# Kernel optimization log

Measured on AMD Instinct MI355X. Metric: run time of the kernel, lower is better.

## Reference

```python
import jax, jax.numpy as jnp
import numpy as np

WBITS = 4
ABITS = 8
OBITS = 8


def fwht(x):
    """Normalized fast Walsh-Hadamard transform along the last axis (n power of 2).
    Equivalent to matmul_hadU with had_K = I, K = 1 (n = 4096 = 2^12)."""
    shape = x.shape
    n = shape[-1]
    x = x.reshape(-1, n)
    h = 1
    while h < n:
        x = x.reshape(-1, n // (2 * h), 2, h)
        a, b = x[:, :, 0, :], x[:, :, 1, :]
        x = jnp.concatenate([a + b, a - b], axis=-1).reshape(-1, n)
        h *= 2
    inv_sqrt_n = jnp.asarray(1.0 / np.sqrt(n), x.dtype)
    return (x * inv_sqrt_n).reshape(shape)


def sym_fake_quant(t, bits, axis):
    """Symmetric min-max RTN fake quantization (per-channel for weights,
    per-token for activations)."""
    qmax = jnp.asarray(2.0 ** (bits - 1) - 1.0, t.dtype)
    scale = jnp.max(jnp.abs(t), axis=axis, keepdims=True) / qmax
    scale = jnp.maximum(scale, jnp.asarray(1e-8, t.dtype))
    q = jnp.clip(jnp.round(t / scale), -qmax, qmax)
    return q * scale


def setup_inputs() -> dict:
    key = jax.random.key(0)
    k1, k2, k3 = jax.random.split(key, 3)
    B, S, DIN, DOUT = 4, 2048, 4096, 4096
    return {
        "input": jax.random.normal(k1, (B, S, DIN), dtype=jnp.float32),
        "weight": jax.random.normal(k2, (DOUT, DIN), dtype=jnp.float32) * 0.02,
        "bias": jax.random.normal(k3, (DOUT,), dtype=jnp.float32) * 0.01,
    }


def reference(input, weight, bias):
    # online full Hadamard rotation of activations
    x = fwht(input)
    # activation quant (per-token, symmetric int8 fake-quant)
    x = sym_fake_quant(x, ABITS, axis=-1)
    # weight quant (per-output-channel, symmetric int4 fake-quant)
    w = sym_fake_quant(weight, WBITS, axis=-1)
    # F.linear: x @ w.T + b
    out = jnp.einsum("bsi,oi->bso", x, w) + bias
    # output quant (per-token, symmetric int8 fake-quant)
    out = sym_fake_quant(out, OBITS, axis=-1)
    return out
```

## Files before the change

kernel.cpp:

```cpp
#include <hip/hip_runtime.h>
#include <hip/hip_bf16.h>

#define DIN 4096
#define DOUT 4096
#define NROWS 8192

typedef int i32x4 __attribute__((ext_vector_type(4)));
typedef int i32x16 __attribute__((ext_vector_type(16)));

__device__ __forceinline__ float block_absmax(float m, float* red) {
  #pragma unroll
  for (int off = 32; off > 0; off >>= 1)
    m = fmaxf(m, __shfl_down(m, off));
  const int tid = threadIdx.x;
  if ((tid & 63) == 0) red[tid >> 6] = m;
  __syncthreads();
  return fmaxf(fmaxf(red[0], red[1]), fmaxf(red[2], red[3]));
}

__global__ __launch_bounds__(256) void fwht_quant_kernel(
    const float* __restrict__ in, char* __restrict__ qx,
    float* __restrict__ sx) {
  __shared__ float lds[4352];
  __shared__ float red[4];
  const int tid = threadIdx.x;
  const size_t row = blockIdx.x;
  const int th = tid >> 4, tl = tid & 15;
  float v[16];

  const float4* src = (const float4*)(in + row * DIN);
  #pragma unroll
  for (int k = 0; k < 4; ++k) {
    float4 f = src[tid * 4 + k];
    v[4 * k + 0] = f.x; v[4 * k + 1] = f.y;
    v[4 * k + 2] = f.z; v[4 * k + 3] = f.w;
  }
  #pragma unroll
  for (int hb = 1; hb < 16; hb <<= 1)
    #pragma unroll
    for (int j = 0; j < 16; ++j)
      if (!(j & hb)) {
        float a0 = v[j], b0 = v[j | hb];
        v[j] = a0 + b0; v[j | hb] = a0 - b0;
      }
  #pragma unroll
  for (int j = 0; j < 16; ++j) lds[17 * tid + j] = v[j];
  __syncthreads();
  #pragma unroll
  for (int j = 0; j < 16; ++j) v[j] = lds[272 * th + 17 * j + tl];
  #pragma unroll
  for (int hb = 1; hb < 16; hb <<= 1)
    #pragma unroll
    for (int j = 0; j < 16; ++j)
      if (!(j & hb)) {
        float a0 = v[j], b0 = v[j | hb];
        v[j] = a0 + b0; v[j | hb] = a0 - b0;
      }
  #pragma unroll
  for (int j = 0; j < 16; ++j) lds[272 * th + 17 * j + tl] = v[j];
  __syncthreads();
  #pragma unroll
  for (int j = 0; j < 16; ++j) v[j] = lds[272 * j + 17 * th + tl];
  #pragma unroll
  for (int hb = 1; hb < 16; hb <<= 1)
    #pragma unroll
    for (int j = 0; j < 16; ++j)
      if (!(j & hb)) {
        float a0 = v[j], b0 = v[j | hb];
        v[j] = a0 + b0; v[j | hb] = a0 - b0;
      }
  float m = 0.0f;
  #pragma unroll
  for (int j = 0; j < 16; ++j) m = fmaxf(m, fabsf(v[j]));
  #pragma unroll
  for (int j = 0; j < 16; ++j) lds[272 * j + 17 * th + tl] = v[j];
  float mx = block_absmax(m, red) * 0.015625f;
  float scale = fmaxf(mx / 127.0f, 1e-8f);
  if (tid == 0) sx[row] = scale;
  const float rs = 1.0f / scale;
  char pk[16];
  #pragma unroll
  for (int j = 0; j < 16; ++j) {
    float q = fminf(fmaxf(rintf((lds[17 * tid + j] * 0.015625f) * rs), -127.f),
                    127.f);
    pk[j] = (char)q;
  }
  *(int4*)(qx + row * DIN + (size_t)tid * 16) = *(const int4*)pk;
}

__global__ __launch_bounds__(256) void wquant_kernel(
    const float* __restrict__ w, char* __restrict__ qw,
    float* __restrict__ sw) {
  __shared__ float buf[DIN];
  __shared__ float red[4];
  const int tid = threadIdx.x;
  const size_t row = blockIdx.x;
  const float4* src = (const float4*)(w + row * DIN);
  float4* b4 = (float4*)buf;
  float m = 0.0f;
  for (int i = tid; i < DIN / 4; i += 256) {
    float4 v = src[i];
    b4[i] = v;
    m = fmaxf(m, fmaxf(fmaxf(fabsf(v.x), fabsf(v.y)),
                       fmaxf(fabsf(v.z), fabsf(v.w))));
  }
  float mx = block_absmax(m, red);
  float scale = fmaxf(mx / 7.0f, 1e-8f);
  if (tid == 0) sw[row] = scale;
  char* dst = qw + row * DIN;
  const float rs = 1.0f / scale;
  for (int i0 = tid * 4; i0 < DIN; i0 += 1024) {
    char4 pk;
    float q0 = fminf(fmaxf(rintf(buf[i0 + 0] * rs), -7.f), 7.f);
    float q1 = fminf(fmaxf(rintf(buf[i0 + 1] * rs), -7.f), 7.f);
    float q2 = fminf(fmaxf(rintf(buf[i0 + 2] * rs), -7.f), 7.f);
    float q3 = fminf(fmaxf(rintf(buf[i0 + 3] * rs), -7.f), 7.f);
    pk.x = (char)q0; pk.y = (char)q1; pk.z = (char)q2; pk.w = (char)q3;
    *(char4*)(dst + i0) = pk;
  }
}

__global__ __launch_bounds__(512, 2) void gemm_kernel(
    const char* __restrict__ A,
    const char* __restrict__ Bt,
    const float* __restrict__ sx, const float* __restrict__ sw,
    const float* __restrict__ bias, float* __restrict__ out) {
  __shared__ char lds[131072];
  const int tid = threadIdx.x;
  const int lane = tid & 63;
  const int wid = tid >> 6;
  const int wr = wid >> 2;
  const int wc = wid & 3;
  const int lh = lane >> 5;
  const int l31 = lane & 31;
  int bid = blockIdx.x;
  int swz = (bid & 7) * 64 + (bid >> 3);
  const size_t row0 = (size_t)(swz >> 4) * 256;
  const size_t col0 = (size_t)(swz & 15) * 256;

  i32x16 acc[4][2] = {};
  i32x4 faA[4], faB[4];
  i32x4 fb[2][4];

#define STAGE(MAT, GROW0, KT, LBASE)                                          \
  {                                                                           \
    _Pragma("unroll")                                                         \
    for (int j = 0; j < 2; ++j) {                                             \
      int chunk = j * 8 + wid;                                                \
      int rr = chunk * 8 + (lane >> 3);                                       \
      int cc = (KT) * 128 + (((lane & 7) ^ (lane >> 3)) << 4);                \
      const char* src = (MAT) + ((GROW0) + rr) * (size_t)DIN + cc;            \
      __builtin_amdgcn_global_load_lds(                                       \
          (const __attribute__((address_space(1))) void*)src,                 \
          (__attribute__((address_space(3))) void*)(lds + (LBASE) +           \
                                                    chunk * 1024),            \
          16, 0, 0);                                                          \
    }                                                                         \
  }
#define STAGE_A(P, HALF, KT) \
  STAGE(A, row0 + (HALF) * 128, KT, (P) * 32768 + (HALF) * 16384)
#define STAGE_B(P, HALF, KT) \
  STAGE(Bt, col0 + (HALF) * 128, KT, 65536 + (P) * 32768 + (HALF) * 16384)

#define DS_FA(DST, Q, P)                                                      \
  {                                                                           \
    int ar_ = (Q) * 64 + wr * 32 + l31;                                       \
    _Pragma("unroll")                                                         \
    for (int kk = 0; kk < 4; ++kk)                                            \
      DST[kk] = *(const i32x4*)(lds + (P) * 32768 + ar_ * 128 +               \
                                (((kk * 2 + lh) ^ (ar_ & 7)) << 4));          \
  }
#define DS_FB(P)                                                              \
  {                                                                           \
    _Pragma("unroll")                                                         \
    for (int nn = 0; nn < 2; ++nn) {                                          \
      int br_ = wc * 64 + nn * 32 + l31;                                      \
      _Pragma("unroll")                                                       \
      for (int kk = 0; kk < 4; ++kk)                                          \
        fb[nn][kk] = *(const i32x4*)(lds + 65536 + (P) * 32768 + br_ * 128 +  \
                                     (((kk * 2 + lh) ^ (br_ & 7)) << 4));     \
    }                                                                         \
  }
#define MFMA8(Q, FA)                                                          \
  {                                                                           \
    __builtin_amdgcn_s_setprio(1);                                            \
    _Pragma("unroll")                                                         \
    for (int kk = 0; kk < 4; ++kk)                                            \
      _Pragma("unroll")                                                       \
      for (int nn = 0; nn < 2; ++nn)                                          \
        acc[Q][nn] = __builtin_amdgcn_mfma_i32_32x32x32_i8(                   \
            fb[nn][kk], FA[kk], acc[Q][nn], 0, 0, 0);                         \
    __builtin_amdgcn_s_setprio(0);                                            \
  }
#define BAR() __builtin_amdgcn_s_barrier()
#define SCHED0() __builtin_amdgcn_sched_barrier(0)

  STAGE_B(0, 0, 0); STAGE_B(0, 1, 0); STAGE_A(0, 0, 0); STAGE_A(0, 1, 0);
  STAGE_B(1, 0, 1); STAGE_B(1, 1, 1); STAGE_A(1, 0, 1);
  asm volatile("s_waitcnt vmcnt(6)" ::: "memory");
  BAR();
  DS_FA(faA, 0, 0);

  #pragma unroll 1
  for (int i = 0; i < 16; ++i) {
    const int a = 2 * i, b = 2 * i + 1;
    const bool nl = (i < 15);
    DS_FB(0);
    DS_FA(faB, 1, 0);
    STAGE_A(1, 1, b);
    SCHED0();
    MFMA8(0, faA);
    BAR();
    DS_FA(faA, 2, 0);
    if (nl) STAGE_B(0, 0, a + 2);
    SCHED0();
    MFMA8(1, faB);
    BAR();
    DS_FA(faB, 3, 0);
    if (nl) STAGE_B(0, 1, a + 2);
    SCHED0();
    MFMA8(2, faA);
    if (nl) { asm volatile("s_waitcnt vmcnt(4)" ::: "memory"); }
    else    { asm volatile("s_waitcnt vmcnt(0)" ::: "memory"); }
    BAR();
    DS_FA(faA, 0, 1);
    if (nl) STAGE_A(0, 0, a + 2);
    SCHED0();
    MFMA8(3, faB);
    BAR();
    DS_FB(1);
    DS_FA(faB, 1, 1);
    if (nl) STAGE_A(0, 1, a + 2);
    SCHED0();
    MFMA8(0, faA);
    BAR();
    DS_FA(faA, 2, 1);
    if (nl) STAGE_B(1, 0, b + 2);
    SCHED0();
    MFMA8(1, faB);
    BAR();
    DS_FA(faB, 3, 1);
    if (nl) STAGE_B(1, 1, b + 2);
    SCHED0();
    MFMA8(2, faA);
    if (nl) { asm volatile("s_waitcnt vmcnt(4)" ::: "memory"); }
    BAR();
    if (nl) { DS_FA(faA, 0, 0); STAGE_A(1, 0, b + 2); }
    SCHED0();
    MFMA8(3, faB);
    BAR();
  }

  #pragma unroll
  for (int q = 0; q < 4; ++q) {
    size_t gr = row0 + q * 64 + wr * 32 + l31;
    float sxr = sx[gr];
    float* orow = out + gr * DOUT;
    #pragma unroll
    for (int nn = 0; nn < 2; ++nn) {
      #pragma unroll
      for (int r4 = 0; r4 < 4; ++r4) {
        size_t gc0 = col0 + wc * 64 + nn * 32 + 8 * r4 + 4 * lh;
        float4 swv = *(const float4*)(sw + gc0);
        float4 bv = *(const float4*)(bias + gc0);
        float4 o;
        o.x = (float)acc[q][nn][r4 * 4 + 0] * (sxr * swv.x) + bv.x;
        o.y = (float)acc[q][nn][r4 * 4 + 1] * (sxr * swv.y) + bv.y;
        o.z = (float)acc[q][nn][r4 * 4 + 2] * (sxr * swv.z) + bv.z;
        o.w = (float)acc[q][nn][r4 * 4 + 3] * (sxr * swv.w) + bv.w;
        *(float4*)(orow + gc0) = o;
      }
    }
  }
#undef STAGE
#undef STAGE_A
#undef STAGE_B
#undef DS_FA
#undef DS_FB
#undef MFMA8
#undef BAR
#undef SCHED0
}

__global__ __launch_bounds__(256) void rowquant_kernel(float* __restrict__ out) {
  __shared__ float red[4];
  const int tid = threadIdx.x;
  const size_t row = blockIdx.x;
  float4* g4 = (float4*)(out + row * DOUT);
  float4 v[4];
  float m = 0.0f;
  #pragma unroll
  for (int k = 0; k < 4; ++k) {
    v[k] = g4[tid + k * 256];
    m = fmaxf(m, fmaxf(fmaxf(fabsf(v[k].x), fabsf(v[k].y)),
                       fmaxf(fabsf(v[k].z), fabsf(v[k].w))));
  }
  float mx = block_absmax(m, red);
  float scale = fmaxf(mx / 127.0f, 1e-8f);
  #pragma unroll
  for (int k = 0; k < 4; ++k) {
    float4 w = v[k];
    w.x = fminf(fmaxf(rintf(w.x / scale), -127.0f), 127.0f) * scale;
    w.y = fminf(fmaxf(rintf(w.y / scale), -127.0f), 127.0f) * scale;
    w.z = fminf(fmaxf(rintf(w.z / scale), -127.0f), 127.0f) * scale;
    w.w = fminf(fmaxf(rintf(w.w / scale), -127.0f), 127.0f) * scale;
    g4[tid + k * 256] = w;
  }
}

extern "C" void kernel_launch(void* const* d_in, const int* in_sizes, int n_in,
                              void* d_out, int out_size, void* d_ws, size_t ws_size,
                              hipStream_t stream) {
  (void)in_sizes; (void)n_in; (void)out_size; (void)ws_size;
  const float* input = (const float*)d_in[0];
  const float* weight = (const float*)d_in[1];
  const float* bias = (const float*)d_in[2];
  float* out = (float*)d_out;
  char* ws = (char*)d_ws;
  char* qx = ws;
  char* qw = ws + ((size_t)32 << 20);
  float* sx = (float*)(ws + ((size_t)48 << 20));
  float* sw = (float*)(ws + ((size_t)48 << 20) + ((size_t)32 << 10));

  fwht_quant_kernel<<<NROWS, 256, 0, stream>>>(input, qx, sx);
  wquant_kernel<<<DOUT, 256, 0, stream>>>(weight, qw, sw);
  gemm_kernel<<<512, 512, 0, stream>>>(qx, qw, sx, sw, bias, out);
  rowquant_kernel<<<NROWS, 256, 0, stream>>>(out);
}
```

Before: 256.3 us.

## Merge activation and weight quant launches; add explicit LDS waits and barriers in GEMM

The FWHT activation quantization and the weight quantization now run as one launch, with the block index choosing which path a block takes. This removes one launch and the tail gap between the two kernels. In the GEMM main loop, each sched_barrier is replaced by an explicit lgkmcnt wait plus an extra workgroup barrier before every MFMA group, so the LDS fragment reads are waited on at a partial count rather than left to the compiler. The extra barriers may add stalls, and the hand-set lgkmcnt counts must exactly match the number of outstanding LDS and scalar ops or fragments will be read before they arrive.

```diff
diff --git a/kernel.cpp b/kernel.cpp
--- a/kernel.cpp
+++ b/kernel.cpp
@@ -18,105 +18,101 @@
   return fmaxf(fmaxf(red[0], red[1]), fmaxf(red[2], red[3]));
 }
 
-__global__ __launch_bounds__(256) void fwht_quant_kernel(
-    const float* __restrict__ in, char* __restrict__ qx,
-    float* __restrict__ sx) {
+__global__ __launch_bounds__(256) void fused_quant_kernel(
+    const float* __restrict__ in, const float* __restrict__ w,
+    char* __restrict__ qx, char* __restrict__ qw,
+    float* __restrict__ sx, float* __restrict__ sw) {
   __shared__ float lds[4352];
   __shared__ float red[4];
   const int tid = threadIdx.x;
-  const size_t row = blockIdx.x;
-  const int th = tid >> 4, tl = tid & 15;
-  float v[16];
-
-  const float4* src = (const float4*)(in + row * DIN);
-  #pragma unroll
-  for (int k = 0; k < 4; ++k) {
-    float4 f = src[tid * 4 + k];
-    v[4 * k + 0] = f.x; v[4 * k + 1] = f.y;
-    v[4 * k + 2] = f.z; v[4 * k + 3] = f.w;
-  }
-  #pragma unroll
-  for (int hb = 1; hb < 16; hb <<= 1)
-    #pragma unroll
-    for (int j = 0; j < 16; ++j)
-      if (!(j & hb)) {
-        float a0 = v[j], b0 = v[j | hb];
-        v[j] = a0 + b0; v[j | hb] = a0 - b0;
-      }
-  #pragma unroll
-  for (int j = 0; j < 16; ++j) lds[17 * tid + j] = v[j];
-  __syncthreads();
-  #pragma unroll
-  for (int j = 0; j < 16; ++j) v[j] = lds[272 * th + 17 * j + tl];
-  #pragma unroll
-  for (int hb = 1; hb < 16; hb <<= 1)
-    #pragma unroll
-    for (int j = 0; j < 16; ++j)
-      if (!(j & hb)) {
-        float a0 = v[j], b0 = v[j | hb];
-        v[j] = a0 + b0; v[j | hb] = a0 - b0;
-      }
-  #pragma unroll
-  for (int j = 0; j < 16; ++j) lds[272 * th + 17 * j + tl] = v[j];
-  __syncthreads();
-  #pragma unroll
-  for (int j = 0; j < 16; ++j) v[j] = lds[272 * j + 17 * th + tl];
-  #pragma unroll
-  for (int hb = 1; hb < 16; hb <<= 1)
-    #pragma unroll
-    for (int j = 0; j < 16; ++j)
-      if (!(j & hb)) {
-        float a0 = v[j], b0 = v[j | hb];
-        v[j] = a0 + b0; v[j | hb] = a0 - b0;
-      }
-  float m = 0.0f;
-  #pragma unroll
-  for (int j = 0; j < 16; ++j) m = fmaxf(m, fabsf(v[j]));
-  #pragma unroll
-  for (int j = 0; j < 16; ++j) lds[272 * j + 17 * th + tl] = v[j];
-  float mx = block_absmax(m, red) * 0.015625f;
-  float scale = fmaxf(mx / 127.0f, 1e-8f);
-  if (tid == 0) sx[row] = scale;
-  const float rs = 1.0f / scale;
-  char pk[16];
-  #pragma unroll
-  for (int j = 0; j < 16; ++j) {
-    float q = fminf(fmaxf(rintf((lds[17 * tid + j] * 0.015625f) * rs), -127.f),
-                    127.f);
-    pk[j] = (char)q;
-  }
-  *(int4*)(qx + row * DIN + (size_t)tid * 16) = *(const int4*)pk;
-}
-
-__global__ __launch_bounds__(256) void wquant_kernel(
-    const float* __restrict__ w, char* __restrict__ qw,
-    float* __restrict__ sw) {
-  __shared__ float buf[DIN];
-  __shared__ float red[4];
-  const int tid = threadIdx.x;
-  const size_t row = blockIdx.x;
-  const float4* src = (const float4*)(w + row * DIN);
-  float4* b4 = (float4*)buf;
-  float m = 0.0f;
-  for (int i = tid; i < DIN / 4; i += 256) {
-    float4 v = src[i];
-    b4[i] = v;
-    m = fmaxf(m, fmaxf(fmaxf(fabsf(v.x), fabsf(v.y)),
-                       fmaxf(fabsf(v.z), fabsf(v.w))));
-  }
-  float mx = block_absmax(m, red);
-  float scale = fmaxf(mx / 7.0f, 1e-8f);
-  if (tid == 0) sw[row] = scale;
-  char* dst = qw + row * DIN;
-  const float rs = 1.0f / scale;
-  for (int i0 = tid * 4; i0 < DIN; i0 += 1024) {
-    char4 pk;
-    float q0 = fminf(fmaxf(rintf(buf[i0 + 0] * rs), -7.f), 7.f);
-    float q1 = fminf(fmaxf(rintf(buf[i0 + 1] * rs), -7.f), 7.f);
-    float q2 = fminf(fmaxf(rintf(buf[i0 + 2] * rs), -7.f), 7.f);
-    float q3 = fminf(fmaxf(rintf(buf[i0 + 3] * rs), -7.f), 7.f);
-    pk.x = (char)q0; pk.y = (char)q1; pk.z = (char)q2; pk.w = (char)q3;
-    *(char4*)(dst + i0) = pk;
+
+  if (blockIdx.x < NROWS) {
+    const size_t row = blockIdx.x;
+    const int th = tid >> 4, tl = tid & 15;
+    float v[16];
+    const float4* src = (const float4*)(in + row * DIN);
+    #pragma unroll
+    for (int k = 0; k < 4; ++k) {
+      float4 f = src[tid * 4 + k];
+      v[4 * k + 0] = f.x; v[4 * k + 1] = f.y;
+      v[4 * k + 2] = f.z; v[4 * k + 3] = f.w;
+    }
+    #pragma unroll
+    for (int hb = 1; hb < 16; hb <<= 1)
+      #pragma unroll
+      for (int j = 0; j < 16; ++j)
+        if (!(j & hb)) {
+          float a0 = v[j], b0 = v[j | hb];
+          v[j] = a0 + b0; v[j | hb] = a0 - b0;
+        }
+    #pragma unroll
+    for (int j = 0; j < 16; ++j) lds[17 * tid + j] = v[j];
+    __syncthreads();
+    #pragma unroll
+    for (int j = 0; j < 16; ++j) v[j] = lds[272 * th + 17 * j + tl];
+    #pragma unroll
+    for (int hb = 1; hb < 16; hb <<= 1)
+      #pragma unroll
+      for (int j = 0; j < 16; ++j)
+        if (!(j & hb)) {
+          float a0 = v[j], b0 = v[j | hb];
+          v[j] = a0 + b0; v[j | hb] = a0 - b0;
+        }
+    #pragma unroll
+    for (int j = 0; j < 16; ++j) lds[272 * th + 17 * j + tl] = v[j];
+    __syncthreads();
+    #pragma unroll
+    for (int j = 0; j < 16; ++j) v[j] = lds[272 * j + 17 * th + tl];
+    #pragma unroll
+    for (int hb = 1; hb < 16; hb <<= 1)
+      #pragma unroll
+      for (int j = 0; j < 16; ++j)
+        if (!(j & hb)) {
+          float a0 = v[j], b0 = v[j | hb];
+          v[j] = a0 + b0; v[j | hb] = a0 - b0;
+        }
+    float m = 0.0f;
+    #pragma unroll
+    for (int j = 0; j < 16; ++j) m = fmaxf(m, fabsf(v[j]));
+    #pragma unroll
+    for (int j = 0; j < 16; ++j) lds[272 * j + 17 * th + tl] = v[j];
+    float mx = block_absmax(m, red) * 0.015625f;
+    float scale = fmaxf(mx / 127.0f, 1e-8f);
+    if (tid == 0) sx[row] = scale;
+    const float rs = 1.0f / scale;
+    char pk[16];
+    #pragma unroll
+    for (int j = 0; j < 16; ++j) {
+      float q = fminf(fmaxf(rintf((lds[17 * tid + j] * 0.015625f) * rs), -127.f),
+                      127.f);
+      pk[j] = (char)q;
+    }
+    *(int4*)(qx + row * DIN + (size_t)tid * 16) = *(const int4*)pk;
+  } else {
+    const size_t row = blockIdx.x - NROWS;
+    const float4* src = (const float4*)(w + row * DIN);
+    float4* b4 = (float4*)lds;
+    float m = 0.0f;
+    for (int i = tid; i < DIN / 4; i += 256) {
+      float4 v = src[i];
+      b4[i] = v;
+      m = fmaxf(m, fmaxf(fmaxf(fabsf(v.x), fabsf(v.y)),
+                         fmaxf(fabsf(v.z), fabsf(v.w))));
+    }
+    float mx = block_absmax(m, red);
+    float scale = fmaxf(mx / 7.0f, 1e-8f);
+    if (tid == 0) sw[row] = scale;
+    char* dst = qw + row * DIN;
+    const float rs = 1.0f / scale;
+    for (int i0 = tid * 4; i0 < DIN; i0 += 1024) {
+      char4 pk;
+      float q0 = fminf(fmaxf(rintf(lds[i0 + 0] * rs), -7.f), 7.f);
+      float q1 = fminf(fmaxf(rintf(lds[i0 + 1] * rs), -7.f), 7.f);
+      float q2 = fminf(fmaxf(rintf(lds[i0 + 2] * rs), -7.f), 7.f);
+      float q3 = fminf(fmaxf(rintf(lds[i0 + 3] * rs), -7.f), 7.f);
+      pk.x = (char)q0; pk.y = (char)q1; pk.z = (char)q2; pk.w = (char)q3;
+      *(char4*)(dst + i0) = pk;
+    }
   }
 }
 
@@ -193,7 +189,10 @@
     __builtin_amdgcn_s_setprio(0);                                            \
   }
 #define BAR() __builtin_amdgcn_s_barrier()
-#define SCHED0() __builtin_amdgcn_sched_barrier(0)
+#define WAIT_LGKM4() \
+  { asm volatile("s_waitcnt lgkmcnt(4)" ::: "memory"); __builtin_amdgcn_sched_barrier(0); }
+#define WAIT_LGKM0() \
+  { asm volatile("s_waitcnt lgkmcnt(0)" ::: "memory"); __builtin_amdgcn_sched_barrier(0); }
 
   STAGE_B(0, 0, 0); STAGE_B(0, 1, 0); STAGE_A(0, 0, 0); STAGE_A(0, 1, 0);
   STAGE_B(1, 0, 1); STAGE_B(1, 1, 1); STAGE_A(1, 0, 1);
@@ -208,45 +207,48 @@
     DS_FB(0);
     DS_FA(faB, 1, 0);
     STAGE_A(1, 1, b);
-    SCHED0();
+    asm volatile("s_waitcnt lgkmcnt(8)" ::: "memory");
+    BAR(); WAIT_LGKM4();
     MFMA8(0, faA);
     BAR();
     DS_FA(faA, 2, 0);
     if (nl) STAGE_B(0, 0, a + 2);
-    SCHED0();
+    BAR(); WAIT_LGKM4();
     MFMA8(1, faB);
     BAR();
     DS_FA(faB, 3, 0);
     if (nl) STAGE_B(0, 1, a + 2);
-    SCHED0();
+    BAR(); WAIT_LGKM4();
     MFMA8(2, faA);
     if (nl) { asm volatile("s_waitcnt vmcnt(4)" ::: "memory"); }
     else    { asm volatile("s_waitcnt vmcnt(0)" ::: "memory"); }
     BAR();
     DS_FA(faA, 0, 1);
     if (nl) STAGE_A(0, 0, a + 2);
-    SCHED0();
+    BAR(); WAIT_LGKM4();
     MFMA8(3, faB);
     BAR();
     DS_FB(1);
     DS_FA(faB, 1, 1);
     if (nl) STAGE_A(0, 1, a + 2);
-    SCHED0();
+    asm volatile("s_waitcnt lgkmcnt(8)" ::: "memory");
+    BAR(); WAIT_LGKM4();
     MFMA8(0, faA);
     BAR();
     DS_FA(faA, 2, 1);
     if (nl) STAGE_B(1, 0, b + 2);
-    SCHED0();
+    BAR(); WAIT_LGKM4();
     MFMA8(1, faB);
     BAR();
     DS_FA(faB, 3, 1);
     if (nl) STAGE_B(1, 1, b + 2);
-    SCHED0();
+    BAR(); WAIT_LGKM4();
     MFMA8(2, faA);
     if (nl) { asm volatile("s_waitcnt vmcnt(4)" ::: "memory"); }
     BAR();
     if (nl) { DS_FA(faA, 0, 0); STAGE_A(1, 0, b + 2); }
-    SCHED0();
+    BAR();
+    if (nl) { WAIT_LGKM4(); } else { WAIT_LGKM0(); }
     MFMA8(3, faB);
     BAR();
   }
@@ -279,7 +281,8 @@
 #undef DS_FB
 #undef MFMA8
 #undef BAR
-#undef SCHED0
+#undef WAIT_LGKM4
+#undef WAIT_LGKM0
 }
 
 __global__ __launch_bounds__(256) void rowquant_kernel(float* __restrict__ out) {
@@ -322,8 +325,8 @@
   float* sx = (float*)(ws + ((size_t)48 << 20));
   float* sw = (float*)(ws + ((size_t)48 << 20) + ((size_t)32 << 10));
 
-  fwht_quant_kernel<<<NROWS, 256, 0, stream>>>(input, qx, sx);
-  wquant_kernel<<<DOUT, 256, 0, stream>>>(weight, qw, sw);
+  fused_quant_kernel<<<NROWS + DOUT, 256, 0, stream>>>(input, weight, qx, qw,
+                                                       sx, sw);
   gemm_kernel<<<512, 512, 0, stream>>>(qx, qw, sx, sw, bias, out);
   rowquant_kernel<<<NROWS, 256, 0, stream>>>(out);
 }
```

New measurement: 261.0 us. About the same (+1.8%).
